# Kernel optimization log

Measured on AMD Instinct MI355X. Metric: run time of the kernel, lower is better.

Reference implementation:

```python
import jax, jax.numpy as jnp
import numpy as np

N = 50000
E = 800000
IN = 128
HEADS = 4
C = 32  # out_features per head
HC = HEADS * C


def setup_inputs() -> dict:
    key = jax.random.key(0)
    ks = jax.random.split(key, 10)
    s_in = 1.0 / np.sqrt(IN)
    x = jax.random.normal(ks[0], (N, IN), dtype=jnp.float32)
    edge_index = jax.random.randint(ks[1], (2, E), 0, N, dtype=jnp.int64)
    Wq = jax.random.normal(ks[2], (IN, HC), dtype=jnp.float32) * s_in
    bq = jnp.zeros((HC,), dtype=jnp.float32)
    Wk = jax.random.normal(ks[3], (IN, HC), dtype=jnp.float32) * s_in
    bk = jnp.zeros((HC,), dtype=jnp.float32)
    Wv = jax.random.normal(ks[4], (IN, HC), dtype=jnp.float32) * s_in
    bv = jnp.zeros((HC,), dtype=jnp.float32)
    Wskip = jax.random.normal(ks[5], (IN, HC), dtype=jnp.float32) * s_in
    bskip = jnp.zeros((HC,), dtype=jnp.float32)
    return {"x": x, "edge_index": edge_index, "Wq": Wq, "bq": bq,
            "Wk": Wk, "bk": bk, "Wv": Wv, "bv": bv,
            "Wskip": Wskip, "bskip": bskip}


def reference(x, edge_index, Wq, bq, Wk, bk, Wv, bv, Wskip, bskip):
    src = edge_index[0]  # message source j
    dst = edge_index[1]  # message target i

    q = (x @ Wq + bq).reshape(N, HEADS, C)
    k = (x @ Wk + bk).reshape(N, HEADS, C)
    v = (x @ Wv + bv).reshape(N, HEADS, C)

    # per-edge attention logits: [E, H]
    logits = jnp.einsum('ehc,ehc->eh', q[dst], k[src]) / jnp.sqrt(
        jnp.asarray(C, dtype=x.dtype))

    # segment softmax over incoming edges of each target node
    seg_max = jax.ops.segment_max(logits, dst, num_segments=N)
    seg_max = jnp.where(jnp.isfinite(seg_max), seg_max, 0.0)
    expd = jnp.exp(logits - seg_max[dst])
    seg_sum = jax.ops.segment_sum(expd, dst, num_segments=N)
    alpha = expd / (seg_sum[dst] + 1e-16)  # [E, H]

    # scatter-add weighted values: [N, H, C]
    msgs = alpha[:, :, None] * v[src]
    out = jax.ops.segment_sum(msgs, dst, num_segments=N)
    out = out.reshape(N, HC) + (x @ Wskip + bskip)  # root/skip connection

    # LeakyReLU(negative_slope=0.2)
    return jnp.where(out >= 0, out, 0.2 * out)
```

## Files before the change

kernel.cpp:

```cpp
#include <hip/hip_runtime.h>

#define N_NODES 50000
#define E_EDGES 800000
#define IN_F 128
#define HC 128
#define ROWTILES 3125
#define PACK_BLOCKS 32
#define GEMM_BLOCKS 1563
#define CAP 64

typedef __attribute__((ext_vector_type(8))) short short8;
typedef __attribute__((ext_vector_type(4))) float floatx4;

__device__ __forceinline__ unsigned short f2bf(float f) {
    union { float f; unsigned u; } x; x.f = f;
    unsigned r = x.u + 0x7FFF + ((x.u >> 16) & 1);
    return (unsigned short)(r >> 16);
}
__device__ __forceinline__ float bflo(unsigned u) {
    union { unsigned u; float f; } c; c.u = u << 16; return c.f;
}
__device__ __forceinline__ float bfhi(unsigned u) {
    union { unsigned u; float f; } c; c.u = u & 0xFFFF0000u; return c.f;
}
__device__ __forceinline__ int swzb(int b) { return b ^ (((b >> 10) & 3) << 5); }
__device__ __forceinline__ int swzf(int b) { return b ^ (((b >> 11) & 3) << 5); }

__global__ __launch_bounds__(256) void pack_w(
    const float* __restrict__ Wq, const float* __restrict__ Wk,
    const float* __restrict__ Wv, const float* __restrict__ Ws,
    const float* __restrict__ bq, const float* __restrict__ bk,
    const float* __restrict__ bv, const float* __restrict__ bs,
    short* __restrict__ bpack, float* __restrict__ bcat,
    int* __restrict__ cnt)
{
    int t = blockIdx.x * 256 + threadIdx.x;
    int lane = t & 63, ks = (t >> 6) & 3, nt = t >> 8;
    int col = nt * 16 + (lane & 15);
    int sec = col >> 7, c = col & 127;
    const float* W = sec == 0 ? Wq : sec == 1 ? Wk : sec == 2 ? Wv : Ws;
    int kbase = ks * 32 + (lane >> 4) * 8;
    short8 b;
#pragma unroll
    for (int j = 0; j < 8; j++) b[j] = (short)f2bf(W[(size_t)(kbase + j) * HC + c]);
    *(short8*)(bpack + (size_t)t * 8) = b;
    if (t < 512) {
        int s2 = t >> 7, c2 = t & 127;
        bcat[t] = (s2 == 0 ? bq : s2 == 1 ? bk : s2 == 2 ? bv : bs)[c2];
    }
    for (int i = t; i < N_NODES; i += PACK_BLOCKS * 256) cnt[i] = 0;
}

__global__ __launch_bounds__(512) void hist_k(
    const int* __restrict__ src, const int* __restrict__ dst,
    int* __restrict__ cnt, int* __restrict__ ssrc)
{
    int e = blockIdx.x * 512 + threadIdx.x;
    if (e < E_EDGES) {
        int d = dst[e];
        int r = atomicAdd(&cnt[d], 1);
        if (r < CAP) ssrc[(size_t)d * CAP + r] = src[e];
    }
}

__global__ __launch_bounds__(256) void gemm_k(
    const float* __restrict__ x, const short* __restrict__ bpack,
    const float* __restrict__ bcat,
    unsigned short* __restrict__ q, unsigned short* __restrict__ k,
    unsigned short* __restrict__ v, float* __restrict__ out)
{
    __shared__ __align__(16) unsigned char lds[2 * 20480];

    const int cg = threadIdx.x >> 6;
    const int lane = threadIdx.x & 63;
    const int l16 = lane & 15, kh = lane >> 4;
    const int rt0 = blockIdx.x * 2;
    const bool has1 = (rt0 + 1) < ROWTILES;

    short8 a[2][4];
#pragma unroll
    for (int t = 0; t < 2; t++) {
        const size_t row = (size_t)(t && has1 ? rt0 + 1 : rt0) * 16 + l16;
#pragma unroll
        for (int ks = 0; ks < 4; ks++) {
            const float* p0 = x + row * IN_F + ks * 32 + kh * 8;
            float4 lo = *(const float4*)p0;
            float4 hi = *(const float4*)(p0 + 4);
            short8 aa;
            aa[0] = (short)f2bf(lo.x); aa[1] = (short)f2bf(lo.y);
            aa[2] = (short)f2bf(lo.z); aa[3] = (short)f2bf(lo.w);
            aa[4] = (short)f2bf(hi.x); aa[5] = (short)f2bf(hi.y);
            aa[6] = (short)f2bf(hi.z); aa[7] = (short)f2bf(hi.w);
            a[t][ks] = aa;
        }
    }

    float bias[8];
#pragma unroll
    for (int n = 0; n < 8; n++) bias[n] = bcat[cg * 128 + n * 16 + l16];

    unsigned char* E0b = lds + cg * 4096;
    unsigned char* E1b = lds + 20480 + cg * 4096;
    unsigned char* E0f = lds + 12288;
    unsigned char* E1f = lds + 20480 + 12288;

    const int ntb = cg * 8;
    short8 bc[4], bn[4];
#pragma unroll
    for (int ks = 0; ks < 4; ks++)
        bc[ks] = *(const short8*)(bpack + ((size_t)(ntb * 4 + ks) * 64 + lane) * 8);

#pragma unroll 1
    for (int nt8 = 0; nt8 < 8; nt8++) {
        if (nt8 < 7) {
#pragma unroll
            for (int ks = 0; ks < 4; ks++)
                bn[ks] = *(const short8*)(bpack + ((size_t)((ntb + nt8 + 1) * 4 + ks) * 64 + lane) * 8);
        }
        floatx4 acc0 = {0.f, 0.f, 0.f, 0.f}, acc1 = {0.f, 0.f, 0.f, 0.f};
#pragma unroll
        for (int ks = 0; ks < 4; ks++) {
            acc0 = __builtin_amdgcn_mfma_f32_16x16x32_bf16(a[0][ks], bc[ks], acc0, 0, 0, 0);
            acc1 = __builtin_amdgcn_mfma_f32_16x16x32_bf16(a[1][ks], bc[ks], acc1, 0, 0, 0);
        }
        const float bs_ = bias[nt8];
        if (cg < 3) {
#pragma unroll
            for (int r = 0; r < 4; r++) {
                int boff = ((kh * 4 + r) * 128 + nt8 * 16 + l16) * 2;
                *(unsigned short*)(E0b + swzb(boff)) = f2bf(acc0[r] + bs_);
                *(unsigned short*)(E1b + swzb(boff)) = f2bf(acc1[r] + bs_);
            }
        } else {
#pragma unroll
            for (int r = 0; r < 4; r++) {
                int boff = ((kh * 4 + r) * 128 + nt8 * 16 + l16) * 4;
                *(float*)(E0f + swzf(boff)) = acc0[r] + bs_;
                *(float*)(E1f + swzf(boff)) = acc1[r] + bs_;
            }
        }
#pragma unroll
        for (int ks = 0; ks < 4; ks++) bc[ks] = bn[ks];
    }

    if (cg < 3) {
        unsigned short* base = (cg == 0) ? q : (cg == 1) ? k : v;
        unsigned short* g0 = base + (size_t)rt0 * 16 * HC;
#pragma unroll
        for (int i = 0; i < 4; i++) {
            int idx = i * 64 + lane;
            *(uint4*)(g0 + idx * 8) = *(const uint4*)(E0b + swzb(idx * 16));
        }
        if (has1) {
            unsigned short* g1 = base + (size_t)(rt0 + 1) * 16 * HC;
#pragma unroll
            for (int i = 0; i < 4; i++) {
                int idx = i * 64 + lane;
                *(uint4*)(g1 + idx * 8) = *(const uint4*)(E1b + swzb(idx * 16));
            }
        }
    } else {
        float* g0 = out + (size_t)rt0 * 16 * HC;
#pragma unroll
        for (int i = 0; i < 8; i++) {
            int idx = i * 64 + lane;
            *(float4*)(g0 + idx * 4) = *(const float4*)(E0f + swzf(idx * 16));
        }
        if (has1) {
            float* g1 = out + (size_t)(rt0 + 1) * 16 * HC;
#pragma unroll
            for (int i = 0; i < 8; i++) {
                int idx = i * 64 + lane;
                *(float4*)(g1 + idx * 4) = *(const float4*)(E1f + swzf(idx * 16));
            }
        }
    }
}

__global__ __launch_bounds__(256) void node_attn(
    const unsigned short* __restrict__ q, const unsigned short* __restrict__ k,
    const unsigned short* __restrict__ v, const int* __restrict__ cnt,
    const int* __restrict__ ssrc, float* __restrict__ out)
{
    const int wave = (blockIdx.x * 256 + threadIdx.x) >> 6;
    if (wave >= N_NODES) return;
    const int lane = threadIdx.x & 63;
    const int node = wave;

    union { unsigned u; float f; } cv;
    const unsigned uq = *(const unsigned*)(q + (size_t)node * HC + lane * 2);
    cv.u = uq << 16;          float qx = cv.f;
    cv.u = uq & 0xFFFF0000u;  float qy = cv.f;

    float accx = 0.f, accy = 0.f, ssum = 0.f;
    int deg = __builtin_amdgcn_readfirstlane(cnt[node]);
    if (deg > CAP) deg = CAP;
    const int* sp = ssrc + (size_t)node * CAP;
    const float scale = 0.17677669529663687f;

    int e = 0;
    for (; e + 3 < deg; e += 4) {
        const int j0 = sp[e],     j1 = sp[e + 1];
        const int j2 = sp[e + 2], j3 = sp[e + 3];
        const unsigned uk0 = *(const unsigned*)(k + (size_t)j0 * HC + lane * 2);
        const unsigned uk1 = *(const unsigned*)(k + (size_t)j1 * HC + lane * 2);
        const unsigned uk2 = *(const unsigned*)(k + (size_t)j2 * HC + lane * 2);
        const unsigned uk3 = *(const unsigned*)(k + (size_t)j3 * HC + lane * 2);
        const unsigned uv0 = *(const unsigned*)(v + (size_t)j0 * HC + lane * 2);
        const unsigned uv1 = *(const unsigned*)(v + (size_t)j1 * HC + lane * 2);
        const unsigned uv2 = *(const unsigned*)(v + (size_t)j2 * HC + lane * 2);
        const unsigned uv3 = *(const unsigned*)(v + (size_t)j3 * HC + lane * 2);
        float p0, p1, p2, p3;
        { float kx, ky;
          cv.u = uk0 << 16; kx = cv.f; cv.u = uk0 & 0xFFFF0000u; ky = cv.f;
          p0 = qx * kx + qy * ky;
          cv.u = uk1 << 16; kx = cv.f; cv.u = uk1 & 0xFFFF0000u; ky = cv.f;
          p1 = qx * kx + qy * ky;
          cv.u = uk2 << 16; kx = cv.f; cv.u = uk2 & 0xFFFF0000u; ky = cv.f;
          p2 = qx * kx + qy * ky;
          cv.u = uk3 << 16; kx = cv.f; cv.u = uk3 & 0xFFFF0000u; ky = cv.f;
          p3 = qx * kx + qy * ky; }
#pragma unroll
        for (int off = 1; off <= 8; off <<= 1) {
            p0 += __shfl_xor(p0, off);
            p1 += __shfl_xor(p1, off);
            p2 += __shfl_xor(p2, off);
            p3 += __shfl_xor(p3, off);
        }
        const float w0 = __expf(p0 * scale);
        const float w1 = __expf(p1 * scale);
        const float w2 = __expf(p2 * scale);
        const float w3 = __expf(p3 * scale);
        { float vx, vy;
          cv.u = uv0 << 16; vx = cv.f; cv.u = uv0 & 0xFFFF0000u; vy = cv.f;
          accx += w0 * vx; accy += w0 * vy;
          cv.u = uv1 << 16; vx = cv.f; cv.u = uv1 & 0xFFFF0000u; vy = cv.f;
          accx += w1 * vx; accy += w1 * vy;
          cv.u = uv2 << 16; vx = cv.f; cv.u = uv2 & 0xFFFF0000u; vy = cv.f;
          accx += w2 * vx; accy += w2 * vy;
          cv.u = uv3 << 16; vx = cv.f; cv.u = uv3 & 0xFFFF0000u; vy = cv.f;
          accx += w3 * vx; accy += w3 * vy; }
        ssum += (w0 + w1) + (w2 + w3);
    }
    for (; e < deg; e++) {
        const int j0 = sp[e];
        const unsigned uk0 = *(const unsigned*)(k + (size_t)j0 * HC + lane * 2);
        const unsigned uv0 = *(const unsigned*)(v + (size_t)j0 * HC + lane * 2);
        float kx, ky;
        cv.u = uk0 << 16; kx = cv.f; cv.u = uk0 & 0xFFFF0000u; ky = cv.f;
        float p0 = qx * kx + qy * ky;
        p0 += __shfl_xor(p0, 1);
        p0 += __shfl_xor(p0, 2);
        p0 += __shfl_xor(p0, 4);
        p0 += __shfl_xor(p0, 8);
        const float w0 = __expf(p0 * scale);
        float vx, vy;
        cv.u = uv0 << 16; vx = cv.f; cv.u = uv0 & 0xFFFF0000u; vy = cv.f;
        accx += w0 * vx; accy += w0 * vy;
        ssum += w0;
    }

    const float inv = 1.0f / (ssum + 1e-16f);
    const float2 sk = *(const float2*)(out + (size_t)node * HC + lane * 2);
    float ox = accx * inv + sk.x;
    float oy = accy * inv + sk.y;
    ox = ox >= 0.f ? ox : 0.2f * ox;
    oy = oy >= 0.f ? oy : 0.2f * oy;
    *(float2*)(out + (size_t)node * HC + lane * 2) = make_float2(ox, oy);
}

extern "C" void kernel_launch(void* const* d_in, const int* in_sizes, int n_in,
                              void* d_out, int out_size, void* d_ws, size_t ws_size,
                              hipStream_t stream)
{
    const float* x    = (const float*)d_in[0];
    const int*   ei   = (const int*)d_in[1];
    const float* Wq   = (const float*)d_in[2];
    const float* bq   = (const float*)d_in[3];
    const float* Wk   = (const float*)d_in[4];
    const float* bk   = (const float*)d_in[5];
    const float* Wv   = (const float*)d_in[6];
    const float* bv   = (const float*)d_in[7];
    const float* Wsk  = (const float*)d_in[8];
    const float* bsk  = (const float*)d_in[9];
    float* out = (float*)d_out;

    char* w = (char*)d_ws;
    const size_t NFB = (size_t)N_NODES * HC * sizeof(unsigned short);
    unsigned short* q = (unsigned short*)w;            w += NFB;
    unsigned short* k = (unsigned short*)w;            w += NFB;
    unsigned short* v = (unsigned short*)w;            w += NFB;
    short* bpack = (short*)w;                          w += 8192 * 8 * sizeof(short);
    float* bcat  = (float*)w;                          w += 512 * sizeof(float);
    int* cnt  = (int*)w;                               w += N_NODES * sizeof(int);
    int* ssrc = (int*)w;

    const int* srcIdx = ei;
    const int* dstIdx = ei + E_EDGES;

    pack_w<<<PACK_BLOCKS, 256, 0, stream>>>(Wq, Wk, Wv, Wsk, bq, bk, bv, bsk,
                                            bpack, bcat, cnt);
    hist_k<<<(E_EDGES + 511) / 512, 512, 0, stream>>>(srcIdx, dstIdx, cnt, ssrc);
    gemm_k<<<GEMM_BLOCKS, 256, 0, stream>>>(
        x, bpack, bcat, q, k, v, out);
    node_attn<<<(N_NODES * 64) / 256, 256, 0, stream>>>(q, k, v, cnt, ssrc, out);
}
```

Before: 148.2 us.

## Interleave K and V into one buffer and batch eight edges per iteration

The GEMM epilogue now writes K and V interleaved per node, so each lane gets its K and V pair in a single 8-byte gather instead of two separate 4-byte gathers. The attention loop processes eight neighbours at a time and masks the tail instead of running a scalar remainder loop. This raises memory-level parallelism for the random gathers. In exchange it adds a block-wide barrier and an extra LDS read pass in the GEMM epilogue, and wastes some loads on padded lanes for low-degree nodes.

```diff
diff --git a/kernel.cpp b/kernel.cpp
--- a/kernel.cpp
+++ b/kernel.cpp
@@ -66,8 +66,8 @@
 __global__ __launch_bounds__(256) void gemm_k(
     const float* __restrict__ x, const short* __restrict__ bpack,
     const float* __restrict__ bcat,
-    unsigned short* __restrict__ q, unsigned short* __restrict__ k,
-    unsigned short* __restrict__ v, float* __restrict__ out)
+    unsigned short* __restrict__ q, unsigned* __restrict__ kv,
+    float* __restrict__ out)
 {
     __shared__ __align__(16) unsigned char lds[2 * 20480];
 
@@ -143,23 +143,22 @@
         for (int ks = 0; ks < 4; ks++) bc[ks] = bn[ks];
     }
 
-    if (cg < 3) {
-        unsigned short* base = (cg == 0) ? q : (cg == 1) ? k : v;
-        unsigned short* g0 = base + (size_t)rt0 * 16 * HC;
+    if (cg == 0) {
+        unsigned short* g0 = q + (size_t)rt0 * 16 * HC;
 #pragma unroll
         for (int i = 0; i < 4; i++) {
             int idx = i * 64 + lane;
             *(uint4*)(g0 + idx * 8) = *(const uint4*)(E0b + swzb(idx * 16));
         }
         if (has1) {
-            unsigned short* g1 = base + (size_t)(rt0 + 1) * 16 * HC;
+            unsigned short* g1 = q + (size_t)(rt0 + 1) * 16 * HC;
 #pragma unroll
             for (int i = 0; i < 4; i++) {
                 int idx = i * 64 + lane;
                 *(uint4*)(g1 + idx * 8) = *(const uint4*)(E1b + swzb(idx * 16));
             }
         }
-    } else {
+    } else if (cg == 3) {
         float* g0 = out + (size_t)rt0 * 16 * HC;
 #pragma unroll
         for (int i = 0; i < 8; i++) {
@@ -175,22 +174,41 @@
             }
         }
     }
+
+    __syncthreads();
+
+    if (cg == 1 || (cg == 2 && has1)) {
+        const int tsel = cg - 1;
+        const unsigned char* Ek = lds + tsel * 20480 + 4096;
+        const unsigned char* Ev = lds + tsel * 20480 + 8192;
+        const int rtg = rt0 + tsel;
+        unsigned* gkv = kv + (size_t)rtg * 16 * 64 * 2;
+#pragma unroll
+        for (int i = 0; i < 8; i++) {
+            int u = i * 64 + lane;
+            int row = u >> 5;
+            int c0 = (u & 31) * 2;
+            int boff = row * 256 + c0 * 4;
+            uint2 kp = *(const uint2*)(Ek + swzb(boff));
+            uint2 vp = *(const uint2*)(Ev + swzb(boff));
+            uint4 o; o.x = kp.x; o.y = vp.x; o.z = kp.y; o.w = vp.y;
+            *(uint4*)(gkv + ((size_t)row * 64 + c0) * 2) = o;
+        }
+    }
 }
 
 __global__ __launch_bounds__(256) void node_attn(
-    const unsigned short* __restrict__ q, const unsigned short* __restrict__ k,
-    const unsigned short* __restrict__ v, const int* __restrict__ cnt,
-    const int* __restrict__ ssrc, float* __restrict__ out)
+    const unsigned short* __restrict__ q, const unsigned* __restrict__ kv,
+    const int* __restrict__ cnt, const int* __restrict__ ssrc,
+    float* __restrict__ out)
 {
     const int wave = (blockIdx.x * 256 + threadIdx.x) >> 6;
     if (wave >= N_NODES) return;
     const int lane = threadIdx.x & 63;
     const int node = wave;
 
-    union { unsigned u; float f; } cv;
     const unsigned uq = *(const unsigned*)(q + (size_t)node * HC + lane * 2);
-    cv.u = uq << 16;          float qx = cv.f;
-    cv.u = uq & 0xFFFF0000u;  float qy = cv.f;
+    const float qx = bflo(uq), qy = bfhi(uq);
 
     float accx = 0.f, accy = 0.f, ssum = 0.f;
     int deg = __builtin_amdgcn_readfirstlane(cnt[node]);
@@ -198,66 +216,35 @@
     const int* sp = ssrc + (size_t)node * CAP;
     const float scale = 0.17677669529663687f;
 
-    int e = 0;
-    for (; e + 3 < deg; e += 4) {
-        const int j0 = sp[e],     j1 = sp[e + 1];
-        const int j2 = sp[e + 2], j3 = sp[e + 3];
-        const unsigned uk0 = *(const unsigned*)(k + (size_t)j0 * HC + lane * 2);
-        const unsigned uk1 = *(const unsigned*)(k + (size_t)j1 * HC + lane * 2);
-        const unsigned uk2 = *(const unsigned*)(k + (size_t)j2 * HC + lane * 2);
-        const unsigned uk3 = *(const unsigned*)(k + (size_t)j3 * HC + lane * 2);
-        const unsigned uv0 = *(const unsigned*)(v + (size_t)j0 * HC + lane * 2);
-        const unsigned uv1 = *(const unsigned*)(v + (size_t)j1 * HC + lane * 2);
-        const unsigned uv2 = *(const unsigned*)(v + (size_t)j2 * HC + lane * 2);
-        const unsigned uv3 = *(const unsigned*)(v + (size_t)j3 * HC + lane * 2);
-        float p0, p1, p2, p3;
-        { float kx, ky;
-          cv.u = uk0 << 16; kx = cv.f; cv.u = uk0 & 0xFFFF0000u; ky = cv.f;
-          p0 = qx * kx + qy * ky;
-          cv.u = uk1 << 16; kx = cv.f; cv.u = uk1 & 0xFFFF0000u; ky = cv.f;
-          p1 = qx * kx + qy * ky;
-          cv.u = uk2 << 16; kx = cv.f; cv.u = uk2 & 0xFFFF0000u; ky = cv.f;
-          p2 = qx * kx + qy * ky;
-          cv.u = uk3 << 16; kx = cv.f; cv.u = uk3 & 0xFFFF0000u; ky = cv.f;
-          p3 = qx * kx + qy * ky; }
+    for (int e0 = 0; e0 < deg; e0 += 8) {
+        int jj[8];
+#pragma unroll
+        for (int t = 0; t < 8; t++) {
+            int ee = e0 + t;
+            jj[t] = sp[ee < deg ? ee : 0];
+        }
+        uint2 kvu[8];
+#pragma unroll
+        for (int t = 0; t < 8; t++)
+            kvu[t] = *(const uint2*)(kv + ((size_t)jj[t] * 64 + lane) * 2);
+
+        float p[8];
+#pragma unroll
+        for (int t = 0; t < 8; t++)
+            p[t] = qx * bflo(kvu[t].x) + qy * bfhi(kvu[t].x);
 #pragma unroll
         for (int off = 1; off <= 8; off <<= 1) {
-            p0 += __shfl_xor(p0, off);
-            p1 += __shfl_xor(p1, off);
-            p2 += __shfl_xor(p2, off);
-            p3 += __shfl_xor(p3, off);
-        }
-        const float w0 = __expf(p0 * scale);
-        const float w1 = __expf(p1 * scale);
-        const float w2 = __expf(p2 * scale);
-        const float w3 = __expf(p3 * scale);
-        { float vx, vy;
-          cv.u = uv0 << 16; vx = cv.f; cv.u = uv0 & 0xFFFF0000u; vy = cv.f;
-          accx += w0 * vx; accy += w0 * vy;
-          cv.u = uv1 << 16; vx = cv.f; cv.u = uv1 & 0xFFFF0000u; vy = cv.f;
-          accx += w1 * vx; accy += w1 * vy;
-          cv.u = uv2 << 16; vx = cv.f; cv.u = uv2 & 0xFFFF0000u; vy = cv.f;
-          accx += w2 * vx; accy += w2 * vy;
-          cv.u = uv3 << 16; vx = cv.f; cv.u = uv3 & 0xFFFF0000u; vy = cv.f;
-          accx += w3 * vx; accy += w3 * vy; }
-        ssum += (w0 + w1) + (w2 + w3);
-    }
-    for (; e < deg; e++) {
-        const int j0 = sp[e];
-        const unsigned uk0 = *(const unsigned*)(k + (size_t)j0 * HC + lane * 2);
-        const unsigned uv0 = *(const unsigned*)(v + (size_t)j0 * HC + lane * 2);
-        float kx, ky;
-        cv.u = uk0 << 16; kx = cv.f; cv.u = uk0 & 0xFFFF0000u; ky = cv.f;
-        float p0 = qx * kx + qy * ky;
-        p0 += __shfl_xor(p0, 1);
-        p0 += __shfl_xor(p0, 2);
-        p0 += __shfl_xor(p0, 4);
-        p0 += __shfl_xor(p0, 8);
-        const float w0 = __expf(p0 * scale);
-        float vx, vy;
-        cv.u = uv0 << 16; vx = cv.f; cv.u = uv0 & 0xFFFF0000u; vy = cv.f;
-        accx += w0 * vx; accy += w0 * vy;
-        ssum += w0;
+#pragma unroll
+            for (int t = 0; t < 8; t++) p[t] += __shfl_xor(p[t], off);
+        }
+#pragma unroll
+        for (int t = 0; t < 8; t++) {
+            float wgt = __expf(p[t] * scale);
+            wgt = (e0 + t < deg) ? wgt : 0.f;
+            ssum += wgt;
+            accx += wgt * bflo(kvu[t].y);
+            accy += wgt * bfhi(kvu[t].y);
+        }
     }
 
     const float inv = 1.0f / (ssum + 1e-16f);
@@ -288,8 +275,7 @@
     char* w = (char*)d_ws;
     const size_t NFB = (size_t)N_NODES * HC * sizeof(unsigned short);
     unsigned short* q = (unsigned short*)w;            w += NFB;
-    unsigned short* k = (unsigned short*)w;            w += NFB;
-    unsigned short* v = (unsigned short*)w;            w += NFB;
+    unsigned* kv = (unsigned*)w;                       w += (size_t)N_NODES * 512;
     short* bpack = (short*)w;                          w += 8192 * 8 * sizeof(short);
     float* bcat  = (float*)w;                          w += 512 * sizeof(float);
     int* cnt  = (int*)w;                               w += N_NODES * sizeof(int);
@@ -301,7 +287,6 @@
     pack_w<<<PACK_BLOCKS, 256, 0, stream>>>(Wq, Wk, Wv, Wsk, bq, bk, bv, bsk,
                                             bpack, bcat, cnt);
     hist_k<<<(E_EDGES + 511) / 512, 512, 0, stream>>>(srcIdx, dstIdx, cnt, ssrc);
-    gemm_k<<<GEMM_BLOCKS, 256, 0, stream>>>(
-        x, bpack, bcat, q, k, v, out);
-    node_attn<<<(N_NODES * 64) / 256, 256, 0, stream>>>(q, k, v, cnt, ssrc, out);
-}
+    gemm_k<<<GEMM_BLOCKS, 256, 0, stream>>>(x, bpack, bcat, q, kv, out);
+    node_attn<<<(N_NODES * 64) / 256, 256, 0, stream>>>(q, kv, cnt, ssrc, out);
+}
```

Result: no change. 145.6 us (-1.8%).
